# Kernel tuning notes

Hardware: AMD Instinct MI355X
Metric: run time of the kernel (lower is better)

Reference implementation:

```python
import jax, jax.numpy as jnp
import numpy as np

B, T, D, R = 4, 2048, 1024, 64  # batch, seq_len, hidden_dim, max_relative_position


def setup_inputs() -> dict:
    key = jax.random.key(0)
    ks = jax.random.split(key, 11)
    s = 1.0 / np.sqrt(D)

    def lin(k):
        return (jax.random.normal(k, (D, D), jnp.float32) * s)

    return {
        "repre": jax.random.normal(ks[0], (B, T, D), jnp.float32),
        "mask": jnp.ones((B, T, T), jnp.int32),  # 1 = valid position
        "st_Wq": lin(ks[1]), "st_bq": jnp.zeros((D,), jnp.float32),
        "st_Wk": lin(ks[2]), "st_bk": jnp.zeros((D,), jnp.float32),
        "st_rel": jax.random.normal(ks[3], (2 * R + 1, D), jnp.float32) * 0.02,
        "ed_Wq": lin(ks[4]), "ed_bq": jnp.zeros((D,), jnp.float32),
        "ed_Wk": lin(ks[5]), "ed_bk": jnp.zeros((D,), jnp.float32),
        "ed_rel": jax.random.normal(ks[6], (2 * R + 1, D), jnp.float32) * 0.02,
    }


def _attn_logits(x, Wq, bq, Wk, bk, rel, mask):
    # Single-head attention scores with relative-position key bias (OpenNMT style).
    d = x.shape[-1]
    q = (x @ Wq + bq) * (1.0 / jnp.sqrt(jnp.float32(d)))  # [B,T,D], pre-scaled query
    k = x @ Wk + bk                                        # [B,T,D]
    scores = jnp.einsum('btd,bsd->bts', q, k)              # [B,T,T] content scores
    Tn = x.shape[1]
    Rn = (rel.shape[0] - 1) // 2
    pos = jnp.arange(Tn)
    # relative position matrix: clip(j - i, -R, R) + R  -> [T,T] indices
    idx = jnp.clip(pos[None, :] - pos[:, None], -Rn, Rn) + Rn
    # q . rel_emb for every relative offset, then gather per (i,j):
    # equivalent to einsum('btd,tsd->bts', q, rel[idx]) without the [T,T,D] gather.
    qr = jnp.einsum('btd,rd->btr', q, rel)                 # [B,T,2R+1]
    scores = scores + qr[:, pos[:, None], idx]             # [B,T,T]
    return jnp.where(mask.astype(bool), scores, jnp.float32(-1e18))


def reference(repre, mask, st_Wq, st_bq, st_Wk, st_bk, st_rel,
              ed_Wq, ed_bq, ed_Wk, ed_bk, ed_rel):
    span_st_logits = _attn_logits(repre, st_Wq, st_bq, st_Wk, st_bk, st_rel, mask)
    span_ed_logits = _attn_logits(repre, ed_Wq, ed_bq, ed_Wk, ed_bk, ed_rel, mask)
    return (span_st_logits, span_ed_logits)
```

## Files before the change

kernel.cpp:

```cpp
#include <hip/hip_runtime.h>

constexpr int Bn = 4;
constexpr int Tn = 2048;
constexpr int Dn = 1024;
constexpr int Rn = 64;
constexpr int RELP = 256;
constexpr int QR_STRIDE = 132;

typedef __bf16 bf8 __attribute__((ext_vector_type(8)));
typedef float f32x4 __attribute__((ext_vector_type(4)));

__device__ __forceinline__ unsigned short f2bf(float f) {
    unsigned int u = __float_as_uint(f);
    u += 0x7fffu + ((u >> 16) & 1u);
    return (unsigned short)(u >> 16);
}

#define GLDS(g, l)                                                            \
    __builtin_amdgcn_global_load_lds(                                         \
        (const __attribute__((address_space(1))) void*)(g),                   \
        (__attribute__((address_space(3))) void*)(l), 16, 0, 0)

#define MFMA_BF16(a, b, c) __builtin_amdgcn_mfma_f32_16x16x32_bf16(a, b, c, 0, 0, 0)

#define SBAR()                                                                \
    do {                                                                      \
        __builtin_amdgcn_sched_barrier(0);                                    \
        __builtin_amdgcn_s_barrier();                                         \
    } while (0)

__device__ __forceinline__ void mfma_gemm_256_k32(
    const unsigned short* __restrict__ Ab,
    const unsigned short* __restrict__ Bb,
    f32x4 (&acc)[8][4], unsigned short* As, unsigned short* Bs)
{
    const int tid  = threadIdx.x;
    const int lane = tid & 63, wid = tid >> 6;
    const int wr = wid >> 2, wc = wid & 3;
    const int l15 = lane & 15, lq = lane >> 4;

    const int pc = (((l15 & 1) << 2) | lq) ^ ((l15 >> 1) & 7);
    const int lane_off = ((l15 >> 1) << 6) + (pc << 3);
    const int aoff = wr * 4096 + lane_off;
    const int boff = wc * 2048 + lane_off;

    const int P0 = tid, P1 = tid + 512;
    const int cr0 = P0 >> 3, cr1 = P1 >> 3;
    const int c0 = cr0 * 8 + ((P0 & 7) ^ (cr0 & 7));
    const int c1 = cr1 * 8 + ((P1 & 7) ^ (cr1 & 7));
    const size_t g0 = (size_t)(c0 >> 2) * Dn + (size_t)((c0 & 3) << 3);
    const size_t g1 = (size_t)(c1 >> 2) * Dn + (size_t)((c1 & 3) << 3);
    const int d0 = P0 * 8, d1 = P1 * 8;

#define STAGE(src, buf)                                                       \
    do {                                                                      \
        GLDS((src) + g0, (buf) + d0);                                         \
        GLDS((src) + g1, (buf) + d1);                                         \
    } while (0)

    constexpr int NT = Dn / 32;

    STAGE(Ab, As);
    STAGE(Bb, Bs);
    STAGE(Ab + 32, As + 8192);
    STAGE(Bb + 32, Bs + 8192);
    asm volatile("s_waitcnt vmcnt(4)" ::: "memory");
    SBAR();

    int bufi = 0;
    bf8 a8[8], b4[4];
#pragma unroll 1
    for (int T = 0; T < NT; ++T) {
        const int cb  = bufi << 13;
        const int sb  = (bufi == 0 ? 2 : bufi - 1) << 13;
        const bool st = T < NT - 2;
        const unsigned short* At = Ab + (T + 2) * 32;
        const unsigned short* Bt = Bb + (T + 2) * 32;

#pragma unroll
        for (int m = 0; m < 8; ++m)
            a8[m] = *(const bf8*)&As[cb + aoff + m * 512];
        b4[0] = *(const bf8*)&Bs[cb + boff];
        b4[1] = *(const bf8*)&Bs[cb + boff + 512];
        if (st) STAGE(At, As + sb);
        SBAR();
        __builtin_amdgcn_s_setprio(1);
#pragma unroll
        for (int m = 0; m < 8; ++m) {
            acc[m][0] = MFMA_BF16(a8[m], b4[0], acc[m][0]);
            acc[m][1] = MFMA_BF16(a8[m], b4[1], acc[m][1]);
        }
        __builtin_amdgcn_s_setprio(0);
        SBAR();

        b4[2] = *(const bf8*)&Bs[cb + boff + 1024];
        b4[3] = *(const bf8*)&Bs[cb + boff + 1536];
        if (st) STAGE(Bt, Bs + sb);
        SBAR();
        __builtin_amdgcn_s_setprio(1);
#pragma unroll
        for (int m = 0; m < 8; ++m) {
            acc[m][2] = MFMA_BF16(a8[m], b4[2], acc[m][2]);
            acc[m][3] = MFMA_BF16(a8[m], b4[3], acc[m][3]);
        }
        __builtin_amdgcn_s_setprio(0);
        if (st) {
            asm volatile("s_waitcnt vmcnt(4)" ::: "memory");
        } else if (T == NT - 2) {
            asm volatile("s_waitcnt vmcnt(0)" ::: "memory");
        }
        if (T < NT - 1) SBAR();
        bufi = (bufi == 2) ? 0 : bufi + 1;
    }
#undef STAGE
}

__device__ __forceinline__ void mfma_gemm_128(
    const unsigned short* __restrict__ Ab,
    const unsigned short* __restrict__ Bb,
    int K, f32x4 acc[4][4],
    unsigned short* As, unsigned short* Bs)
{
    const int tid = threadIdx.x;
    const int r0  = tid >> 2;
    const int c8  = (tid & 3) * 8;
    const int lane = tid & 63;
    const int w    = tid >> 6;
    const int wm = (w & 1) * 64, wn = (w >> 1) * 64;
    const int l15 = lane & 15, lq = lane >> 4;

    const int nt = K >> 5;

    GLDS(Ab + (size_t)r0 * K + c8,        As + r0 * 32 + c8);
    GLDS(Ab + ((size_t)r0 + 64) * K + c8, As + (r0 + 64) * 32 + c8);
    GLDS(Bb + (size_t)r0 * K + c8,        Bs + r0 * 32 + c8);
    GLDS(Bb + ((size_t)r0 + 64) * K + c8, Bs + (r0 + 64) * 32 + c8);
    __syncthreads();

    int cur = 0;
    for (int t = 0; t < nt; ++t) {
        if (t + 1 < nt) {
            const int k0 = (t + 1) << 5;
            const int nb = (cur ^ 1) * (128 * 32);
            GLDS(Ab + (size_t)r0 * K + k0 + c8,        As + nb + r0 * 32 + c8);
            GLDS(Ab + ((size_t)r0 + 64) * K + k0 + c8, As + nb + (r0 + 64) * 32 + c8);
            GLDS(Bb + (size_t)r0 * K + k0 + c8,        Bs + nb + r0 * 32 + c8);
            GLDS(Bb + ((size_t)r0 + 64) * K + k0 + c8, Bs + nb + (r0 + 64) * 32 + c8);
        }
        const int cbuf = cur * (128 * 32);
        bf8 a[4], b[4];
#pragma unroll
        for (int i = 0; i < 4; ++i) {
            a[i] = *(const bf8*)&As[cbuf + (wm + i * 16 + l15) * 32 + lq * 8];
            b[i] = *(const bf8*)&Bs[cbuf + (wn + i * 16 + l15) * 32 + lq * 8];
        }
#pragma unroll
        for (int i = 0; i < 4; ++i)
#pragma unroll
            for (int j = 0; j < 4; ++j)
                acc[i][j] = MFMA_BF16(a[i], b[j], acc[i][j]);
        __syncthreads();
        cur ^= 1;
    }
}

__global__ __launch_bounds__(256) void cvt_bf16(
    const float* __restrict__ in, unsigned short* __restrict__ out, int n4)
{
    int i = blockIdx.x * 256 + threadIdx.x;
    if (i < n4) {
        float4 v = ((const float4*)in)[i];
        ushort4 o;
        o.x = f2bf(v.x); o.y = f2bf(v.y); o.z = f2bf(v.z); o.w = f2bf(v.w);
        ((ushort4*)out)[i] = o;
    }
}

__global__ __launch_bounds__(256) void wt_transpose(
    const float* __restrict__ w0, const float* __restrict__ w1,
    const float* __restrict__ w2, const float* __restrict__ w3,
    unsigned short* __restrict__ WT)
{
    __shared__ float t[32][33];
    const int z = blockIdx.z;
    const float* W = z == 0 ? w0 : z == 1 ? w1 : z == 2 ? w2 : w3;
    const int x = blockIdx.x * 32 + threadIdx.x;
    const int y0 = blockIdx.y * 32;
#pragma unroll
    for (int j = 0; j < 32; j += 8)
        t[threadIdx.y + j][threadIdx.x] = W[(size_t)(y0 + threadIdx.y + j) * Dn + x];
    __syncthreads();
    unsigned short* o = WT + (size_t)z * Dn * Dn;
    const int n0 = blockIdx.x * 32;
#pragma unroll
    for (int j = 0; j < 32; j += 8)
        o[(size_t)(n0 + threadIdx.y + j) * Dn + y0 + threadIdx.x] =
            f2bf(t[threadIdx.x][threadIdx.y + j]);
}

__global__ __launch_bounds__(256) void rel_pad(
    const float* __restrict__ st_rel, const float* __restrict__ ed_rel,
    unsigned short* __restrict__ relb)
{
    const int z = blockIdx.y;
    const float* in = z ? ed_rel : st_rel;
    const int i4 = blockIdx.x * 256 + threadIdx.x;
    const int row = (i4 * 4) >> 10;
    const int col = (i4 * 4) & 1023;
    ushort4 o; o.x = 0; o.y = 0; o.z = 0; o.w = 0;
    if (row < 2 * Rn + 1) {
        float4 v = *(const float4*)(in + (size_t)row * 1024 + col);
        o.x = f2bf(v.x); o.y = f2bf(v.y); o.z = f2bf(v.z); o.w = f2bf(v.w);
    }
    ((ushort4*)(relb + (size_t)z * RELP * 1024))[i4] = o;
}

__global__ __launch_bounds__(512, 2) void proj_gemm256(
    const unsigned short* __restrict__ Xb, const unsigned short* __restrict__ Wb,
    const float* __restrict__ b0, const float* __restrict__ b1,
    const float* __restrict__ b2, const float* __restrict__ b3,
    unsigned short* __restrict__ outQK, float qscale)
{
    __shared__ unsigned short As[3 * 8192], Bs[3 * 8192];
    const int z = blockIdx.z;
    const float* bias = z == 0 ? b0 : z == 1 ? b1 : z == 2 ? b2 : b3;
    const float scale = (z & 1) ? 1.0f : qscale;

    const unsigned short* Ab = Xb + (size_t)blockIdx.x * 256 * Dn;
    const unsigned short* Bb = Wb + ((size_t)z * Dn + blockIdx.y * 256) * Dn;

    f32x4 zero = {0.f, 0.f, 0.f, 0.f};
    f32x4 acc[8][4];
#pragma unroll
    for (int i = 0; i < 8; ++i)
#pragma unroll
        for (int j = 0; j < 4; ++j) acc[i][j] = zero;

    mfma_gemm_256_k32(Ab, Bb, acc, As, Bs);

    const int tid = threadIdx.x, lane = tid & 63, wid = tid >> 6;
    const int wr = wid >> 2, wc = wid & 3;
    const int l15 = lane & 15, lq = lane >> 4;
    unsigned short* out = outQK + (size_t)z * (size_t)Bn * Tn * Dn;
    const int row0 = blockIdx.x * 256 + wr * 128 + lq * 4;
    const int col0 = blockIdx.y * 256 + wc * 64 + l15;

#pragma unroll
    for (int ni = 0; ni < 4; ++ni) {
        const int col = col0 + ni * 16;
        const float bvv = bias[col];
#pragma unroll
        for (int mi = 0; mi < 8; ++mi)
#pragma unroll
            for (int r = 0; r < 4; ++r) {
                const int row = row0 + mi * 16 + r;
                out[(size_t)row * Dn + col] = f2bf((acc[mi][ni][r] + bvv) * scale);
            }
    }
}

__global__ __launch_bounds__(256) void qr_gemm(
    const unsigned short* __restrict__ QKb, const unsigned short* __restrict__ relb,
    float* __restrict__ QR)
{
    __shared__ unsigned short As[2 * 128 * 32], Bs[2 * 128 * 32];
    const int z = blockIdx.z;
    const unsigned short* Ab = QKb + ((size_t)(z * 2) * Bn * Tn + blockIdx.x * 128) * Dn;
    const unsigned short* Bb = relb + ((size_t)z * RELP + blockIdx.y * 128) * Dn;

    f32x4 zero = {0.f, 0.f, 0.f, 0.f};
    f32x4 acc[4][4];
#pragma unroll
    for (int i = 0; i < 4; ++i)
#pragma unroll
        for (int j = 0; j < 4; ++j) acc[i][j] = zero;

    mfma_gemm_128(Ab, Bb, Dn, acc, As, Bs);

    const int tid = threadIdx.x, lane = tid & 63, w = tid >> 6;
    const int wm = (w & 1) * 64, wn = (w >> 1) * 64;
    const int l15 = lane & 15, lq = lane >> 4;
    float* out = QR + (size_t)z * (size_t)Bn * Tn * QR_STRIDE;

#pragma unroll
    for (int ni = 0; ni < 4; ++ni) {
        const int col = blockIdx.y * 128 + wn + ni * 16 + l15;
        if (col >= 2 * Rn + 1) continue;
#pragma unroll
        for (int mi = 0; mi < 4; ++mi) {
#pragma unroll
            for (int r = 0; r < 4; ++r) {
                const int row = blockIdx.x * 128 + wm + mi * 16 + lq * 4 + r;
                out[(size_t)row * QR_STRIDE + col] = acc[mi][ni][r];
            }
        }
    }
}

__global__ __launch_bounds__(512, 2) void scores_gemm256(
    const unsigned short* __restrict__ QKb, const float* __restrict__ QR,
    const int* __restrict__ mask, float* __restrict__ Out)
{
    __shared__ unsigned short As[3 * 8192], Bs[3 * 8192];
    const int z = blockIdx.z;
    const int side = z >> 2, bt = z & 3;

    const unsigned short* Ab =
        QKb + ((size_t)side * 2 * Bn * Tn + (size_t)bt * Tn + blockIdx.x * 256) * Dn;
    const unsigned short* Bb =
        QKb + (((size_t)side * 2 + 1) * Bn * Tn + (size_t)bt * Tn + blockIdx.y * 256) * Dn;
    const float* QRb = QR + ((size_t)side * Bn * Tn + (size_t)bt * Tn) * QR_STRIDE;
    const int* maskb = mask + (size_t)bt * Tn * Tn;
    float* outb = Out + ((size_t)side * Bn + bt) * (size_t)Tn * Tn;

    f32x4 zero = {0.f, 0.f, 0.f, 0.f};
    f32x4 acc[8][4];
#pragma unroll
    for (int i = 0; i < 8; ++i)
#pragma unroll
        for (int j = 0; j < 4; ++j) acc[i][j] = zero;

    mfma_gemm_256_k32(Ab, Bb, acc, As, Bs);

    const int tid = threadIdx.x, lane = tid & 63, wid = tid >> 6;
    const int wr = wid >> 2, wc = wid & 3;
    const int l15 = lane & 15, lq = lane >> 4;
    const int i0 = blockIdx.x * 256 + wr * 128 + lq * 4;
    const int j0 = blockIdx.y * 256 + wc * 64 + l15;

#pragma unroll
    for (int mi = 0; mi < 8; ++mi) {
#pragma unroll
        for (int r = 0; r < 4; ++r) {
            const int i = i0 + mi * 16 + r;
            const float* qrow = QRb + (size_t)i * QR_STRIDE;
            const int* mrow = maskb + (size_t)i * Tn;
            float* orow = outb + (size_t)i * Tn;
#pragma unroll
            for (int ni = 0; ni < 4; ++ni) {
                const int j = j0 + ni * 16;
                int d = j - i;
                d = d < -Rn ? -Rn : (d > Rn ? Rn : d);
                const float qv = qrow[d + Rn];
                orow[j] = mrow[j] ? acc[mi][ni][r] + qv : -1e18f;
            }
        }
    }
}

extern "C" void kernel_launch(void* const* d_in, const int* in_sizes, int n_in,
                              void* d_out, int out_size, void* d_ws, size_t ws_size,
                              hipStream_t stream) {
    const float* repre  = (const float*)d_in[0];
    const int*   mask   = (const int*)  d_in[1];
    const float* st_Wq  = (const float*)d_in[2];
    const float* st_bq  = (const float*)d_in[3];
    const float* st_Wk  = (const float*)d_in[4];
    const float* st_bk  = (const float*)d_in[5];
    const float* st_rel = (const float*)d_in[6];
    const float* ed_Wq  = (const float*)d_in[7];
    const float* ed_bq  = (const float*)d_in[8];
    const float* ed_Wk  = (const float*)d_in[9];
    const float* ed_bk  = (const float*)d_in[10];
    const float* ed_rel = (const float*)d_in[11];
    float* out = (float*)d_out;

    const size_t MT = (size_t)Bn * Tn;

    unsigned short* Xb   = (unsigned short*)d_ws;
    unsigned short* Wb   = Xb + MT * Dn;
    unsigned short* relb = Wb + (size_t)4 * Dn * Dn;
    unsigned short* QKb  = relb + (size_t)2 * RELP * Dn;
    float* QRbuf = (float*)(QKb + (size_t)4 * MT * Dn);

    const float qscale = 0.03125f;
    dim3 blk(256);

    {
        int n4 = (int)(MT * Dn / 4);
        cvt_bf16<<<dim3((n4 + 255) / 256), blk, 0, stream>>>(repre, Xb, n4);
        wt_transpose<<<dim3(32, 32, 4), dim3(32, 8), 0, stream>>>(
            st_Wq, st_Wk, ed_Wq, ed_Wk, Wb);
        rel_pad<<<dim3(RELP * Dn / 4 / 256, 2), blk, 0, stream>>>(st_rel, ed_rel, relb);
    }

    proj_gemm256<<<dim3((int)MT / 256, Dn / 256, 4), dim3(512), 0, stream>>>(
        Xb, Wb, st_bq, st_bk, ed_bq, ed_bk, QKb, qscale);

    qr_gemm<<<dim3((int)MT / 128, RELP / 128, 2), blk, 0, stream>>>(QKb, relb, QRbuf);

    scores_gemm256<<<dim3(Tn / 256, Tn / 256, 8), dim3(512), 0, stream>>>(
        QKb, QRbuf, mask, out);
}
```

Baseline: 569.7 us.

## Bit-pack mask and switch 256-tile GEMM to double-buffered LDS pipeline

A new kernel packs the int32 mask into a bitmask, written into the now-unused bf16 input buffer. The scores epilogue then reads one bit per element instead of a 4-byte int, which cuts epilogue mask traffic, though the mask is still read once in full by the packing pass. The GEMM core goes from a 3-stage LDS ring with split MFMA phases to a simpler 2-buffer scheme with one barrier per k-step. Launch bounds are raised to 4 waves per SIMD to try for higher occupancy, at the risk of register pressure with 32 accumulators and less latency hiding from the shallower prefetch.

```diff
diff --git a/kernel.cpp b/kernel.cpp
--- a/kernel.cpp
+++ b/kernel.cpp
@@ -22,12 +22,6 @@
         (__attribute__((address_space(3))) void*)(l), 16, 0, 0)
 
 #define MFMA_BF16(a, b, c) __builtin_amdgcn_mfma_f32_16x16x32_bf16(a, b, c, 0, 0, 0)
-
-#define SBAR()                                                                \
-    do {                                                                      \
-        __builtin_amdgcn_sched_barrier(0);                                    \
-        __builtin_amdgcn_s_barrier();                                         \
-    } while (0)
 
 __device__ __forceinline__ void mfma_gemm_256_k32(
     const unsigned short* __restrict__ Ab,
@@ -62,55 +56,35 @@
 
     STAGE(Ab, As);
     STAGE(Bb, Bs);
-    STAGE(Ab + 32, As + 8192);
-    STAGE(Bb + 32, Bs + 8192);
-    asm volatile("s_waitcnt vmcnt(4)" ::: "memory");
-    SBAR();
-
-    int bufi = 0;
+    asm volatile("s_waitcnt vmcnt(0)" ::: "memory");
+    __builtin_amdgcn_s_barrier();
+
     bf8 a8[8], b4[4];
 #pragma unroll 1
     for (int T = 0; T < NT; ++T) {
-        const int cb  = bufi << 13;
-        const int sb  = (bufi == 0 ? 2 : bufi - 1) << 13;
-        const bool st = T < NT - 2;
-        const unsigned short* At = Ab + (T + 2) * 32;
-        const unsigned short* Bt = Bb + (T + 2) * 32;
-
+        const int cb = (T & 1) << 13;
+        const int sb = cb ^ 8192;
+        if (T + 1 < NT) {
+            STAGE(Ab + (T + 1) * 32, As + sb);
+            STAGE(Bb + (T + 1) * 32, Bs + sb);
+        }
 #pragma unroll
         for (int m = 0; m < 8; ++m)
             a8[m] = *(const bf8*)&As[cb + aoff + m * 512];
-        b4[0] = *(const bf8*)&Bs[cb + boff];
-        b4[1] = *(const bf8*)&Bs[cb + boff + 512];
-        if (st) STAGE(At, As + sb);
-        SBAR();
+#pragma unroll
+        for (int n = 0; n < 4; ++n)
+            b4[n] = *(const bf8*)&Bs[cb + boff + n * 512];
         __builtin_amdgcn_s_setprio(1);
 #pragma unroll
-        for (int m = 0; m < 8; ++m) {
-            acc[m][0] = MFMA_BF16(a8[m], b4[0], acc[m][0]);
-            acc[m][1] = MFMA_BF16(a8[m], b4[1], acc[m][1]);
-        }
+        for (int m = 0; m < 8; ++m)
+#pragma unroll
+            for (int n = 0; n < 4; ++n)
+                acc[m][n] = MFMA_BF16(a8[m], b4[n], acc[m][n]);
         __builtin_amdgcn_s_setprio(0);
-        SBAR();
-
-        b4[2] = *(const bf8*)&Bs[cb + boff + 1024];
-        b4[3] = *(const bf8*)&Bs[cb + boff + 1536];
-        if (st) STAGE(Bt, Bs + sb);
-        SBAR();
-        __builtin_amdgcn_s_setprio(1);
-#pragma unroll
-        for (int m = 0; m < 8; ++m) {
-            acc[m][2] = MFMA_BF16(a8[m], b4[2], acc[m][2]);
-            acc[m][3] = MFMA_BF16(a8[m], b4[3], acc[m][3]);
-        }
-        __builtin_amdgcn_s_setprio(0);
-        if (st) {
-            asm volatile("s_waitcnt vmcnt(4)" ::: "memory");
-        } else if (T == NT - 2) {
+        __builtin_amdgcn_sched_barrier(0);
+        if (T + 1 < NT)
             asm volatile("s_waitcnt vmcnt(0)" ::: "memory");
-        }
-        if (T < NT - 1) SBAR();
-        bufi = (bufi == 2) ? 0 : bufi + 1;
+        __builtin_amdgcn_s_barrier();
     }
 #undef STAGE
 }
@@ -215,13 +189,22 @@
     ((ushort4*)(relb + (size_t)z * RELP * 1024))[i4] = o;
 }
 
-__global__ __launch_bounds__(512, 2) void proj_gemm256(
+__global__ __launch_bounds__(256) void mask_pack(
+    const int* __restrict__ mask, unsigned long long* __restrict__ pm)
+{
+    const int g = blockIdx.x * 256 + threadIdx.x;
+    const int v = mask[g];
+    unsigned long long b = __ballot(v != 0);
+    if ((threadIdx.x & 63) == 0) pm[g >> 6] = b;
+}
+
+__global__ __launch_bounds__(512, 4) void proj_gemm256(
     const unsigned short* __restrict__ Xb, const unsigned short* __restrict__ Wb,
     const float* __restrict__ b0, const float* __restrict__ b1,
     const float* __restrict__ b2, const float* __restrict__ b3,
     unsigned short* __restrict__ outQK, float qscale)
 {
-    __shared__ unsigned short As[3 * 8192], Bs[3 * 8192];
+    __shared__ unsigned short As[2 * 8192], Bs[2 * 8192];
     const int z = blockIdx.z;
     const float* bias = z == 0 ? b0 : z == 1 ? b1 : z == 2 ? b2 : b3;
     const float scale = (z & 1) ? 1.0f : qscale;
@@ -297,11 +280,11 @@
     }
 }
 
-__global__ __launch_bounds__(512, 2) void scores_gemm256(
+__global__ __launch_bounds__(512, 4) void scores_gemm256(
     const unsigned short* __restrict__ QKb, const float* __restrict__ QR,
-    const int* __restrict__ mask, float* __restrict__ Out)
-{
-    __shared__ unsigned short As[3 * 8192], Bs[3 * 8192];
+    const unsigned int* __restrict__ pmask, float* __restrict__ Out)
+{
+    __shared__ unsigned short As[2 * 8192], Bs[2 * 8192];
     const int z = blockIdx.z;
     const int side = z >> 2, bt = z & 3;
 
@@ -310,7 +293,7 @@
     const unsigned short* Bb =
         QKb + (((size_t)side * 2 + 1) * Bn * Tn + (size_t)bt * Tn + blockIdx.y * 256) * Dn;
     const float* QRb = QR + ((size_t)side * Bn * Tn + (size_t)bt * Tn) * QR_STRIDE;
-    const int* maskb = mask + (size_t)bt * Tn * Tn;
+    const unsigned int* pmb = pmask + (size_t)bt * Tn * (Tn / 32);
     float* outb = Out + ((size_t)side * Bn + bt) * (size_t)Tn * Tn;
 
     f32x4 zero = {0.f, 0.f, 0.f, 0.f};
@@ -334,7 +317,7 @@
         for (int r = 0; r < 4; ++r) {
             const int i = i0 + mi * 16 + r;
             const float* qrow = QRb + (size_t)i * QR_STRIDE;
-            const int* mrow = maskb + (size_t)i * Tn;
+            const unsigned int* mwrow = pmb + (size_t)i * (Tn / 32);
             float* orow = outb + (size_t)i * Tn;
 #pragma unroll
             for (int ni = 0; ni < 4; ++ni) {
@@ -342,7 +325,9 @@
                 int d = j - i;
                 d = d < -Rn ? -Rn : (d > Rn ? Rn : d);
                 const float qv = qrow[d + Rn];
-                orow[j] = mrow[j] ? acc[mi][ni][r] + qv : -1e18f;
+                const unsigned int mw = mwrow[j >> 5];
+                const bool ok = (mw >> (j & 31)) & 1u;
+                orow[j] = ok ? acc[mi][ni][r] + qv : -1e18f;
             }
         }
     }
@@ -372,6 +357,7 @@
     unsigned short* relb = Wb + (size_t)4 * Dn * Dn;
     unsigned short* QKb  = relb + (size_t)2 * RELP * Dn;
     float* QRbuf = (float*)(QKb + (size_t)4 * MT * Dn);
+    unsigned long long* pmask = (unsigned long long*)Xb;
 
     const float qscale = 0.03125f;
     dim3 blk(256);
@@ -387,8 +373,11 @@
     proj_gemm256<<<dim3((int)MT / 256, Dn / 256, 4), dim3(512), 0, stream>>>(
         Xb, Wb, st_bq, st_bk, ed_bq, ed_bk, QKb, qscale);
 
+    mask_pack<<<dim3((int)(Bn * (size_t)Tn * Tn / 256)), blk, 0, stream>>>(
+        mask, pmask);
+
     qr_gemm<<<dim3((int)MT / 128, RELP / 128, 2), blk, 0, stream>>>(QKb, relb, QRbuf);
 
     scores_gemm256<<<dim3(Tn / 256, Tn / 256, 8), dim3(512), 0, stream>>>(
-        QKb, QRbuf, mask, out);
-}
+        QKb, QRbuf, (const unsigned int*)pmask, out);
+}
```

Result: slower. 1.666 ms (+192.5%).
